# Optimization experiments

Hardware: AMD Instinct MI355X
Metric: run time of the kernel (lower is better)

The kernel has to match this reference:

```python
import jax, jax.numpy as jnp
import numpy as np

B, IN, OUT, F, COMP = 8192, 4096, 4096, 16, 1024
FS = IN // F  # fragment_size = 256


def setup_inputs() -> dict:
    key = jax.random.key(0)
    k1, k2, k3, k4, k5 = jax.random.split(key, 5)
    x = jax.random.normal(k1, (B, IN), dtype=jnp.float32)
    selector_weights = jax.random.normal(k2, (F, FS), dtype=jnp.float32) / np.sqrt(FS)
    expert_weights = jax.random.normal(k3, (F, FS, OUT), dtype=jnp.float32) / np.sqrt(FS)
    # nn.Linear default init ~ U(-1/sqrt(fan_in), 1/sqrt(fan_in)); scale is irrelevant for correctness
    W_comp = jax.random.normal(k4, (COMP, IN), dtype=jnp.float32) / np.sqrt(IN)
    W_net = jax.random.normal(k5, (OUT, COMP), dtype=jnp.float32) / np.sqrt(COMP)
    return {"x": x, "selector_weights": selector_weights, "expert_weights": expert_weights,
            "W_comp": W_comp, "W_net": W_net}


def reference(x, selector_weights, expert_weights, W_comp, W_net):
    # Training-mode forward: soft top-fragment gating + dense compress path.
    b, in_f = x.shape
    f, fs = selector_weights.shape
    xf = x.reshape(b, f, fs)                                  # [B, F, FS]
    scores = jnp.einsum('bfi,fi->bf', xf, selector_weights)   # [B, F]
    probs = jax.nn.softmax(scores, axis=1)                    # [B, F]
    # gated grouped matmul: sum_f probs[b,f] * (x_f @ W_f)
    expert_out = jnp.einsum('bfi,fio,bf->bo', xf, expert_weights, probs)  # [B, OUT]
    # mask = 1 - probs expanded per-feature (fragment_mapping = repeat_interleave)
    mask = 1.0 - jnp.repeat(probs, fs, axis=1)                # [B, IN]
    masked = x * mask
    compressed = masked @ W_comp.T                            # [B, COMP]
    out = compressed @ W_net.T + expert_out                   # [B, OUT]
    return out
```

## Files before the change

### kernel.cpp

```cpp
#include <hip/hip_runtime.h>
#include <hip/hip_bf16.h>
#include <cstdint>
#include <cstddef>

#define B_    8192
#define IN_   4096
#define OUT_  4096
#define F_    16
#define FS_   256
#define COMP_ 1024
#define KBIG  (IN_ + COMP_)

typedef unsigned short ushort_t;
typedef __attribute__((ext_vector_type(8))) short short8;
typedef __attribute__((ext_vector_type(4))) float f32x4;

__device__ __forceinline__ ushort_t f2b(float f) {
  unsigned u = __float_as_uint(f);
  u += 0x7fffu + ((u >> 16) & 1u);
  return (ushort_t)(u >> 16);
}

__device__ __forceinline__ void gll16(const void* gp, void* lp) {
  __builtin_amdgcn_global_load_lds(
      (const __attribute__((address_space(1))) unsigned int*)gp,
      (__attribute__((address_space(3))) unsigned int*)lp, 16, 0, 0);
}

__global__ void __launch_bounds__(256) gate_kernel(
    const float* __restrict__ x, const float* __restrict__ sel,
    ushort_t* __restrict__ Abig, ushort_t* __restrict__ Mbuf) {
  const int row = blockIdx.x;
  const int t = threadIdx.x;
  const float* xr = x + (size_t)row * IN_ + t * 16;
  float4 xv0 = ((const float4*)xr)[0];
  float4 xv1 = ((const float4*)xr)[1];
  float4 xv2 = ((const float4*)xr)[2];
  float4 xv3 = ((const float4*)xr)[3];

  const int f = t >> 4;
  const int sub = t & 15;
  const float* sp = sel + f * FS_ + sub * 16;
  float4 s0 = ((const float4*)sp)[0];
  float4 s1 = ((const float4*)sp)[1];
  float4 s2 = ((const float4*)sp)[2];
  float4 s3 = ((const float4*)sp)[3];

  float dot = xv0.x * s0.x + xv0.y * s0.y + xv0.z * s0.z + xv0.w * s0.w
            + xv1.x * s1.x + xv1.y * s1.y + xv1.z * s1.z + xv1.w * s1.w
            + xv2.x * s2.x + xv2.y * s2.y + xv2.z * s2.z + xv2.w * s2.w
            + xv3.x * s3.x + xv3.y * s3.y + xv3.z * s3.z + xv3.w * s3.w;

  #pragma unroll
  for (int off = 8; off; off >>= 1) dot += __shfl_xor(dot, off, 64);

  __shared__ float sc[F_];
  if (sub == 0) sc[f] = dot;
  __syncthreads();

  float mx = sc[0];
  #pragma unroll
  for (int i = 1; i < F_; ++i) mx = fmaxf(mx, sc[i]);
  float sum = 0.f;
  #pragma unroll
  for (int i = 0; i < F_; ++i) sum += __expf(sc[i] - mx);
  const float p = __expf(sc[f] - mx) / sum;

  float xs[16] = {xv0.x, xv0.y, xv0.z, xv0.w, xv1.x, xv1.y, xv1.z, xv1.w,
                  xv2.x, xv2.y, xv2.z, xv2.w, xv3.x, xv3.y, xv3.z, xv3.w};
  union { ushort_t u[8]; uint4 v; } a0, a1, m0, m1;
  #pragma unroll
  for (int j = 0; j < 8; ++j) {
    float y0 = xs[j] * p;
    float y1 = xs[8 + j] * p;
    a0.u[j] = f2b(y0);
    a1.u[j] = f2b(y1);
    m0.u[j] = f2b(xs[j] - y0);
    m1.u[j] = f2b(xs[8 + j] - y1);
  }
  ushort_t* ap = Abig + (size_t)row * KBIG + t * 16;
  *(uint4*)ap = a0.v;
  *(uint4*)(ap + 8) = a1.v;
  ushort_t* mp = Mbuf + (size_t)row * IN_ + t * 16;
  *(uint4*)mp = m0.v;
  *(uint4*)(mp + 8) = m1.v;
}

__global__ void __launch_bounds__(256) conv_expertT(
    const float* __restrict__ We, ushort_t* __restrict__ Bbig) {
  __shared__ float tile[64][65];
  const int k0 = blockIdx.x * 64;
  const int o0 = blockIdx.y * 64;
  const int t = threadIdx.x;
  const int kr = t >> 4;
  const int oq = t & 15;
  #pragma unroll
  for (int rr = 0; rr < 4; ++rr) {
    int k = rr * 16 + kr;
    float4 v = *(const float4*)(We + (size_t)(k0 + k) * OUT_ + o0 + oq * 4);
    tile[k][oq * 4 + 0] = v.x;
    tile[k][oq * 4 + 1] = v.y;
    tile[k][oq * 4 + 2] = v.z;
    tile[k][oq * 4 + 3] = v.w;
  }
  __syncthreads();
  const int kc = t & 7;
  #pragma unroll
  for (int rr = 0; rr < 2; ++rr) {
    int o = rr * 32 + (t >> 3);
    union { ushort_t u[8]; uint4 v; } w;
    #pragma unroll
    for (int j = 0; j < 8; ++j) w.u[j] = f2b(tile[kc * 8 + j][o]);
    *(uint4*)(Bbig + (size_t)(o0 + o) * KBIG + k0 + kc * 8) = w.v;
  }
}

__global__ void __launch_bounds__(256) conv_net(
    const float* __restrict__ Wnet, ushort_t* __restrict__ Bbig) {
  int tid = blockIdx.x * 256 + threadIdx.x;
  int base = tid * 8;
  int o = base >> 10;
  int c = base & (COMP_ - 1);
  float4 v0 = ((const float4*)(Wnet + base))[0];
  float4 v1 = ((const float4*)(Wnet + base))[1];
  union { ushort_t u[8]; uint4 v; } w;
  w.u[0] = f2b(v0.x); w.u[1] = f2b(v0.y); w.u[2] = f2b(v0.z); w.u[3] = f2b(v0.w);
  w.u[4] = f2b(v1.x); w.u[5] = f2b(v1.y); w.u[6] = f2b(v1.z); w.u[7] = f2b(v1.w);
  *(uint4*)(Bbig + (size_t)o * KBIG + IN_ + c) = w.v;
}

__global__ void __launch_bounds__(256) conv_comp(
    const float* __restrict__ Wc, ushort_t* __restrict__ Wcb) {
  int tid = blockIdx.x * 256 + threadIdx.x;
  int base = tid * 8;
  float4 v0 = ((const float4*)(Wc + base))[0];
  float4 v1 = ((const float4*)(Wc + base))[1];
  union { ushort_t u[8]; uint4 v; } w;
  w.u[0] = f2b(v0.x); w.u[1] = f2b(v0.y); w.u[2] = f2b(v0.z); w.u[3] = f2b(v0.w);
  w.u[4] = f2b(v1.x); w.u[5] = f2b(v1.y); w.u[6] = f2b(v1.z); w.u[7] = f2b(v1.w);
  *(uint4*)(Wcb + base) = w.v;
}

__global__ void __launch_bounds__(256) reduce_split(
    const float* __restrict__ p0, const float* __restrict__ p1,
    ushort_t* __restrict__ Abig) {
  int tid = blockIdx.x * 256 + threadIdx.x;
  float4 a = ((const float4*)p0)[tid];
  float4 b = ((const float4*)p1)[tid];
  int row = tid >> 8;
  int c4 = tid & 255;
  union { ushort_t u[4]; uint2 v; } w;
  w.u[0] = f2b(a.x + b.x);
  w.u[1] = f2b(a.y + b.y);
  w.u[2] = f2b(a.z + b.z);
  w.u[3] = f2b(a.w + b.w);
  *(uint2*)(Abig + (size_t)row * KBIG + IN_ + c4 * 4) = w.v;
}

template <bool BF16_OUT>
__global__ void __launch_bounds__(256, 4) gemm_bt(
    const ushort_t* __restrict__ A, int lda,
    const ushort_t* __restrict__ Bt, int ldb,
    int KS, void* __restrict__ Cp, int ldc, int num_pid_n,
    int num_pid, size_t coff) {
  __shared__ __align__(16) ushort_t As[128 * 64];
  __shared__ __align__(16) ushort_t Bs[128 * 64];
  const int t = threadIdx.x;
  const int wave = t >> 6;
  const int lane = t & 63;
  const int wr = (wave >> 1) * 64;
  const int wc = (wave & 1) * 64;
  const int r = lane & 15;
  const int q = lane >> 4;

  const int s = blockIdx.x / num_pid;
  const int rem_all = blockIdx.x - s * num_pid;
  A += (size_t)s * KS;
  Bt += (size_t)s * KS;

  const int pids_per_group = num_pid_n << 4;
  const int group_id = rem_all / pids_per_group;
  const int rem = rem_all - group_id * pids_per_group;
  const int pid_m = (group_id << 4) + (rem & 15);
  const int pid_n = rem >> 4;

  const int srow = wave * 8 + (lane >> 3);
  const int gch = (lane & 7) ^ ((lane >> 3) & 7);
  const ushort_t* ga = A + (size_t)(pid_m * 128 + srow) * lda + gch * 8;
  const ushort_t* gb = Bt + (size_t)(pid_n * 128 + srow) * ldb + gch * 8;
  const size_t a32 = (size_t)32 * lda;
  const size_t b32 = (size_t)32 * ldb;

  f32x4 acc[4][4] = {};

  for (int kk = 0; kk < KS; kk += 64) {
    #pragma unroll
    for (int rA = 0; rA < 4; ++rA)
      gll16(ga + rA * a32, As + rA * 2048 + wave * 512);
    #pragma unroll
    for (int rB = 0; rB < 4; ++rB)
      gll16(gb + rB * b32, Bs + rB * 2048 + wave * 512);
    ga += 64;
    gb += 64;
    __syncthreads();

    #pragma unroll
    for (int ks = 0; ks < 2; ++ks) {
      short8 af[4], bfr[4];
      #pragma unroll
      for (int mi = 0; mi < 4; ++mi) {
        const int row = wr + mi * 16 + r;
        af[mi] = *(const short8*)(As + row * 64 + (((ks * 4 + q) ^ (r & 7)) * 8));
      }
      #pragma unroll
      for (int ni = 0; ni < 4; ++ni) {
        const int row = wc + ni * 16 + r;
        bfr[ni] = *(const short8*)(Bs + row * 64 + (((ks * 4 + q) ^ (r & 7)) * 8));
      }
      #pragma unroll
      for (int mi = 0; mi < 4; ++mi)
        #pragma unroll
        for (int ni = 0; ni < 4; ++ni)
          acc[mi][ni] = __builtin_amdgcn_mfma_f32_16x16x32_bf16(
              af[mi], bfr[ni], acc[mi][ni], 0, 0, 0);
    }
    __syncthreads();
  }

  const int row0 = pid_m * 128 + wr + q * 4;
  const int col0 = pid_n * 128 + wc + r;
  #pragma unroll
  for (int mi = 0; mi < 4; ++mi) {
    #pragma unroll
    for (int ni = 0; ni < 4; ++ni) {
      const int row = row0 + mi * 16;
      const int col = col0 + ni * 16;
      #pragma unroll
      for (int rr = 0; rr < 4; ++rr) {
        float v = acc[mi][ni][rr];
        if (BF16_OUT)
          ((ushort_t*)Cp)[(size_t)(row + rr) * ldc + col + s * coff] = f2b(v);
        else
          ((float*)Cp)[(size_t)(row + rr) * ldc + col + s * coff] = v;
      }
    }
  }
}

extern "C" void kernel_launch(void* const* d_in, const int* in_sizes, int n_in,
                              void* d_out, int out_size, void* d_ws, size_t ws_size,
                              hipStream_t stream) {
  const float* x     = (const float*)d_in[0];
  const float* sel   = (const float*)d_in[1];
  const float* We    = (const float*)d_in[2];
  const float* Wcomp = (const float*)d_in[3];
  const float* Wnet  = (const float*)d_in[4];
  float* out = (float*)d_out;

  char* ws = (char*)d_ws;
  const size_t szAbig = (size_t)B_ * KBIG * 2;
  const size_t szMbuf = (size_t)B_ * IN_ * 2;
  const size_t szBbig = (size_t)OUT_ * KBIG * 2;
  ushort_t* Abig = (ushort_t*)ws;
  ushort_t* Mbuf = (ushort_t*)(ws + szAbig);
  ushort_t* Bbig = (ushort_t*)(ws + szAbig + szMbuf);
  ushort_t* Wcb  = (ushort_t*)(ws + szAbig + szMbuf + szBbig);

  float* part0 = out;
  float* part1 = out + (size_t)B_ * COMP_;

  gate_kernel<<<B_, 256, 0, stream>>>(x, sel, Abig, Mbuf);

  conv_expertT<<<dim3(IN_ / 64, OUT_ / 64), 256, 0, stream>>>(We, Bbig);
  conv_net<<<(OUT_ * COMP_) / (256 * 8), 256, 0, stream>>>(Wnet, Bbig);
  conv_comp<<<(COMP_ * IN_) / (256 * 8), 256, 0, stream>>>(Wcomp, Wcb);

  gemm_bt<false><<<2 * (B_ / 128) * (COMP_ / 128), 256, 0, stream>>>(
      Mbuf, IN_, Wcb, IN_, IN_ / 2, (void*)part0, COMP_, COMP_ / 128,
      (B_ / 128) * (COMP_ / 128), (size_t)B_ * COMP_);
  reduce_split<<<(B_ * COMP_) / (256 * 4), 256, 0, stream>>>(part0, part1, Abig);

  gemm_bt<false><<<(B_ / 128) * (OUT_ / 128), 256, 0, stream>>>(
      Abig, KBIG, Bbig, KBIG, KBIG, (void*)out, OUT_, OUT_ / 128,
      (B_ / 128) * (OUT_ / 128), 0);
}
```

Before: 739.5 us.

## Replace 128x128 GEMM with 256x256 double-buffered pipelined 8-wave kernel

Replaces the single-buffered 128x128 bf16 MFMA GEMM with a 256x256-tile, 512-thread kernel. The new kernel double-buffers LDS and interleaves the global-to-LDS loads for the next K tiles with MFMA phases, using explicit waitcnt and barriers plus s_setprio. It also remaps block IDs with an XCD-aware swizzle. The aim is more operand reuse per tile and load latency hidden behind compute, in exchange for 128KB of LDS per block, fewer blocks in flight, and complex hand-scheduled synchronization.

```diff
diff --git a/kernel.cpp b/kernel.cpp
--- a/kernel.cpp
+++ b/kernel.cpp
@@ -158,25 +158,23 @@
 }
 
 template <bool BF16_OUT>
-__global__ void __launch_bounds__(256, 4) gemm_bt(
+__global__ void __launch_bounds__(512, 2) gemm256(
     const ushort_t* __restrict__ A, int lda,
     const ushort_t* __restrict__ Bt, int ldb,
     int KS, void* __restrict__ Cp, int ldc, int num_pid_n,
     int num_pid, size_t coff) {
-  __shared__ __align__(16) ushort_t As[128 * 64];
-  __shared__ __align__(16) ushort_t Bs[128 * 64];
+  __shared__ __align__(16) ushort_t As[2 * 256 * 64];
+  __shared__ __align__(16) ushort_t Bs[2 * 256 * 64];
   const int t = threadIdx.x;
   const int wave = t >> 6;
   const int lane = t & 63;
-  const int wr = (wave >> 1) * 64;
-  const int wc = (wave & 1) * 64;
-  const int r = lane & 15;
-  const int q = lane >> 4;
 
   const int s = blockIdx.x / num_pid;
-  const int rem_all = blockIdx.x - s * num_pid;
+  int rem_all = blockIdx.x - s * num_pid;
   A += (size_t)s * KS;
   Bt += (size_t)s * KS;
+
+  rem_all = (rem_all & 7) * (num_pid >> 3) + (rem_all >> 3);
 
   const int pids_per_group = num_pid_n << 4;
   const int group_id = rem_all / pids_per_group;
@@ -184,53 +182,132 @@
   const int pid_m = (group_id << 4) + (rem & 15);
   const int pid_n = rem >> 4;
 
-  const int srow = wave * 8 + (lane >> 3);
-  const int gch = (lane & 7) ^ ((lane >> 3) & 7);
-  const ushort_t* ga = A + (size_t)(pid_m * 128 + srow) * lda + gch * 8;
-  const ushort_t* gb = Bt + (size_t)(pid_n * 128 + srow) * ldb + gch * 8;
-  const size_t a32 = (size_t)32 * lda;
-  const size_t b32 = (size_t)32 * ldb;
-
-  f32x4 acc[4][4] = {};
-
-  for (int kk = 0; kk < KS; kk += 64) {
-    #pragma unroll
-    for (int rA = 0; rA < 4; ++rA)
-      gll16(ga + rA * a32, As + rA * 2048 + wave * 512);
-    #pragma unroll
-    for (int rB = 0; rB < 4; ++rB)
-      gll16(gb + rB * b32, Bs + rB * 2048 + wave * 512);
-    ga += 64;
-    gb += 64;
-    __syncthreads();
-
-    #pragma unroll
-    for (int ks = 0; ks < 2; ++ks) {
-      short8 af[4], bfr[4];
-      #pragma unroll
-      for (int mi = 0; mi < 4; ++mi) {
-        const int row = wr + mi * 16 + r;
-        af[mi] = *(const short8*)(As + row * 64 + (((ks * 4 + q) ^ (r & 7)) * 8));
-      }
-      #pragma unroll
-      for (int ni = 0; ni < 4; ++ni) {
-        const int row = wc + ni * 16 + r;
-        bfr[ni] = *(const short8*)(Bs + row * 64 + (((ks * 4 + q) ^ (r & 7)) * 8));
-      }
-      #pragma unroll
-      for (int mi = 0; mi < 4; ++mi)
-        #pragma unroll
-        for (int ni = 0; ni < 4; ++ni)
-          acc[mi][ni] = __builtin_amdgcn_mfma_f32_16x16x32_bf16(
-              af[mi], bfr[ni], acc[mi][ni], 0, 0, 0);
-    }
-    __syncthreads();
-  }
-
-  const int row0 = pid_m * 128 + wr + q * 4;
-  const int col0 = pid_n * 128 + wc + r;
-  #pragma unroll
-  for (int mi = 0; mi < 4; ++mi) {
+  const int wr = (wave >> 2) * 128;
+  const int wc = (wave & 3) * 64;
+
+  const int lr = lane >> 3;
+  const int gch = (lane & 7) ^ lr;
+  const ushort_t* gA = A + (size_t)(pid_m * 256 + wave * 8 + lr) * lda + gch * 8;
+  const ushort_t* gB = Bt + (size_t)(pid_n * 256 + wave * 8 + lr) * ldb + gch * 8;
+  const size_t a64 = (size_t)64 * lda;
+  const size_t b64 = (size_t)64 * ldb;
+  ushort_t* lA = As + wave * 512;
+  ushort_t* lB = Bs + wave * 512;
+
+  #define STAGE_A(BF, H, KT) do {                                          \
+    const ushort_t* g_ = gA + (size_t)(KT) * 64 + (size_t)(2 * (H)) * a64; \
+    ushort_t* d_ = lA + (BF) * 16384 + (H) * 8192;                         \
+    gll16(g_, d_);                                                         \
+    gll16(g_ + a64, d_ + 4096); } while (0)
+  #define STAGE_B(BF, H, KT) do {                                          \
+    const ushort_t* g_ = gB + (size_t)(KT) * 64 + (size_t)(2 * (H)) * b64; \
+    ushort_t* d_ = lB + (BF) * 16384 + (H) * 8192;                         \
+    gll16(g_, d_);                                                         \
+    gll16(g_ + b64, d_ + 4096); } while (0)
+
+  const int r = lane & 15;
+  const int q = lane >> 4;
+  const int sw = r & 7;
+  const int sl0 = (q ^ sw) * 8;
+  const int sl1 = ((q + 4) ^ sw) * 8;
+  const ushort_t* aRd = As + (wr >> 7) * 8192 + r * 64;
+  const ushort_t* bRd = Bs + (wc >> 7) * 8192 + (wc & 64) * 64 + r * 64;
+
+  const int nt = KS >> 6;
+
+  f32x4 acc[8][4] = {};
+  short8 a[4][2], b[4][2];
+
+  #define MFMA_PH(MB, NB) do {                                            \
+    __builtin_amdgcn_s_setprio(1);                                        \
+    _Pragma("unroll")                                                     \
+    for (int mi = 0; mi < 4; ++mi) {                                      \
+      _Pragma("unroll")                                                   \
+      for (int nj = 0; nj < 2; ++nj) {                                    \
+        _Pragma("unroll")                                                 \
+        for (int ks = 0; ks < 2; ++ks)                                    \
+          acc[(MB) + mi][(NB) + nj] =                                     \
+              __builtin_amdgcn_mfma_f32_16x16x32_bf16(                    \
+                  a[mi][ks], b[(NB) + nj][ks], acc[(MB) + mi][(NB) + nj], \
+                  0, 0, 0);                                               \
+      }                                                                   \
+    }                                                                     \
+    __builtin_amdgcn_s_setprio(0); } while (0)
+
+  #define WAIT_LGKM0() do {                                               \
+    asm volatile("s_waitcnt lgkmcnt(0)" ::: "memory");                    \
+    __builtin_amdgcn_sched_barrier(0); } while (0)
+
+  STAGE_A(0, 0, 0); STAGE_A(0, 1, 0);
+  STAGE_B(0, 0, 0); STAGE_B(0, 1, 0);
+  if (nt > 1) {
+    STAGE_B(1, 0, 1); STAGE_B(1, 1, 1);
+    asm volatile("s_waitcnt vmcnt(4)" ::: "memory");
+  } else {
+    asm volatile("s_waitcnt vmcnt(0)" ::: "memory");
+  }
+  __builtin_amdgcn_sched_barrier(0);
+  __builtin_amdgcn_s_barrier();
+
+  for (int kt = 0; kt < nt; ++kt) {
+    const int bf = kt & 1;
+    const int nb = bf ^ 1;
+    const ushort_t* aB = aRd + bf * 16384;
+    const ushort_t* bB = bRd + bf * 16384;
+    const bool p1ok = kt + 1 < nt;
+    const bool p2ok = kt + 2 < nt;
+
+    #pragma unroll
+    for (int mi = 0; mi < 4; ++mi) {
+      a[mi][0] = *(const short8*)(aB + mi * 1024 + sl0);
+      a[mi][1] = *(const short8*)(aB + mi * 1024 + sl1);
+    }
+    #pragma unroll
+    for (int nj = 0; nj < 2; ++nj) {
+      b[nj][0] = *(const short8*)(bB + nj * 1024 + sl0);
+      b[nj][1] = *(const short8*)(bB + nj * 1024 + sl1);
+    }
+    if (p1ok) STAGE_A(nb, 0, kt + 1);
+    __builtin_amdgcn_s_barrier();
+    WAIT_LGKM0();
+    MFMA_PH(0, 0);
+    __builtin_amdgcn_s_barrier();
+
+    #pragma unroll
+    for (int nj = 2; nj < 4; ++nj) {
+      b[nj][0] = *(const short8*)(bB + nj * 1024 + sl0);
+      b[nj][1] = *(const short8*)(bB + nj * 1024 + sl1);
+    }
+    if (p1ok) STAGE_A(nb, 1, kt + 1);
+    __builtin_amdgcn_s_barrier();
+    WAIT_LGKM0();
+    MFMA_PH(0, 2);
+    __builtin_amdgcn_s_barrier();
+
+    #pragma unroll
+    for (int mi = 0; mi < 4; ++mi) {
+      a[mi][0] = *(const short8*)(aB + (mi + 4) * 1024 + sl0);
+      a[mi][1] = *(const short8*)(aB + (mi + 4) * 1024 + sl1);
+    }
+    if (p2ok) STAGE_B(bf, 0, kt + 2);
+    __builtin_amdgcn_s_barrier();
+    WAIT_LGKM0();
+    MFMA_PH(4, 0);
+    __builtin_amdgcn_s_barrier();
+
+    if (p2ok) STAGE_B(bf, 1, kt + 2);
+    __builtin_amdgcn_s_barrier();
+    MFMA_PH(4, 2);
+    if (p2ok) asm volatile("s_waitcnt vmcnt(4)" ::: "memory");
+    else      asm volatile("s_waitcnt vmcnt(0)" ::: "memory");
+    __builtin_amdgcn_sched_barrier(0);
+    __builtin_amdgcn_s_barrier();
+  }
+
+  const int row0 = pid_m * 256 + wr + q * 4;
+  const int col0 = pid_n * 256 + wc + r;
+  #pragma unroll
+  for (int mi = 0; mi < 8; ++mi) {
     #pragma unroll
     for (int ni = 0; ni < 4; ++ni) {
       const int row = row0 + mi * 16;
@@ -245,6 +322,10 @@
       }
     }
   }
+  #undef STAGE_A
+  #undef STAGE_B
+  #undef MFMA_PH
+  #undef WAIT_LGKM0
 }
 
 extern "C" void kernel_launch(void* const* d_in, const int* in_sizes, int n_in,
@@ -275,12 +356,12 @@
   conv_net<<<(OUT_ * COMP_) / (256 * 8), 256, 0, stream>>>(Wnet, Bbig);
   conv_comp<<<(COMP_ * IN_) / (256 * 8), 256, 0, stream>>>(Wcomp, Wcb);
 
-  gemm_bt<false><<<2 * (B_ / 128) * (COMP_ / 128), 256, 0, stream>>>(
-      Mbuf, IN_, Wcb, IN_, IN_ / 2, (void*)part0, COMP_, COMP_ / 128,
-      (B_ / 128) * (COMP_ / 128), (size_t)B_ * COMP_);
+  gemm256<false><<<2 * (B_ / 256) * (COMP_ / 256), 512, 0, stream>>>(
+      Mbuf, IN_, Wcb, IN_, IN_ / 2, (void*)part0, COMP_, COMP_ / 256,
+      (B_ / 256) * (COMP_ / 256), (size_t)B_ * COMP_);
   reduce_split<<<(B_ * COMP_) / (256 * 4), 256, 0, stream>>>(part0, part1, Abig);
 
-  gemm_bt<false><<<(B_ / 128) * (OUT_ / 128), 256, 0, stream>>>(
-      Abig, KBIG, Bbig, KBIG, KBIG, (void*)out, OUT_, OUT_ / 128,
-      (B_ / 128) * (OUT_ / 128), 0);
-}
+  gemm256<false><<<(B_ / 256) * (OUT_ / 256), 512, 0, stream>>>(
+      Abig, KBIG, Bbig, KBIG, KBIG, (void*)out, OUT_, OUT_ / 256,
+      (B_ / 256) * (OUT_ / 256), 0);
+}
```

Result: no change. 725.4 us (-1.9%).
